# Performance work log

Hardware: AMD Instinct MI355X
Metric: run time of the kernel (lower is better)

Reference implementation:

```python
import jax, jax.numpy as jnp
import numpy as np

HIP_L, HIP_R = 11, 12          # hip joint indices along V
K_LIST = (2, 3, 4, 5)          # soft-selector kNN MoE k values
TAU = 0.35                     # tau_center for ball softmax
EPS = 1e-6


def _sym_norm(A):
    # D^{-1/2} A D^{-1/2} without materializing diag matrices
    d = A.sum(-1)
    dis = jax.lax.rsqrt(d + EPS)
    return dis[..., :, None] * A * dis[..., None, :]


def _knn_adj(pos, k):
    # pos: (N, M, 3) -> 0/1 kNN adjacency (+I self loop, diag ends up 2 as in torch ref)
    M = pos.shape[1]
    diff = pos[:, :, None, :] - pos[:, None, :, :]
    d = jnp.sqrt(jnp.sum(diff * diff, axis=-1))  # (N, M, M) euclidean cdist
    idx = jax.lax.top_k(-d, k)[1]                # (N, M, k) k smallest distances (incl. self)
    A = jax.nn.one_hot(idx, M, dtype=pos.dtype).sum(2)  # scatter 1.0 at kNN columns
    return A + jnp.eye(M, dtype=pos.dtype)


def setup_inputs() -> dict:
    key = jax.random.key(0)
    k1, k2 = jax.random.split(key)
    N, C, T, V, M = 64, 8, 300, 17, 12
    x = jax.random.normal(k1, (N, C, T, V, M), jnp.float32)
    alpha_logits = jax.random.normal(k2, (len(K_LIST),), jnp.float32) * 0.1
    lambda_fuse = jnp.array([0.1], jnp.float32)
    tag_gate = jnp.array([1.0], jnp.float32)
    return {"x": x, "alpha_logits": alpha_logits,
            "lambda_fuse": lambda_fuse, "tag_gate": tag_gate}


def reference(x, alpha_logits, lambda_fuse, tag_gate):
    N, C, T, V, M = x.shape
    # hip-root position averaged over time: (N, M, 3)
    root3 = 0.5 * (x[:, 0:3, :, HIP_L, :] + x[:, 0:3, :, HIP_R, :])  # (N,3,T,M)
    pos = root3.mean(2).transpose(0, 2, 1)                           # (N,M,3)

    # kNN mixture-of-graphs, sym-normalized, detached (detach_adj=True)
    A_knn_stack = jnp.stack([_sym_norm(_knn_adj(pos, k)) for k in K_LIST], 1)  # (N,K,M,M)
    A_knn_stack = jax.lax.stop_gradient(A_knn_stack)
    alpha = jax.nn.softmax(alpha_logits)          # global selector, temp=1
    A_knn = jnp.einsum('k,nkij->nij', alpha, A_knn_stack)

    # soft ball-star graph
    s = x[:, 3].mean((1, 2))                      # (N,M) ball score
    p = jax.nn.softmax(s / TAU, axis=1)
    A_ball = p[:, :, None] + p[:, None, :] + jnp.eye(M, dtype=x.dtype)
    A_ball = jax.lax.stop_gradient(_sym_norm(A_ball))

    # adaptive ball weight from confidence of p (NOT detached)
    w = jnp.clip((jnp.max(p, 1, keepdims=True) - 1.0 / M) / (1.0 - 1.0 / M + EPS), 0.0, 1.0)
    A = w[:, :, None] * A_ball + (1.0 - w[:, :, None]) * A_knn  # (N,M,M)

    # message passing across persons on hip-root features, fused back residually
    root = 0.5 * (x[:, :, :, HIP_L, :] + x[:, :, :, HIP_R, :])  # (N,C,T,M)
    agg = jnp.einsum('nuv,nctv->nctu', A, root)                 # (N,C,T,M)
    g = jnp.tanh(tag_gate[0])  # ramp=1 (ramp_epochs=0), gate_max=1
    return x + g * lambda_fuse[0] * (agg - root)[:, :, :, None, :]
```

## Files before the change

### kernel.cpp

```cpp
#include <hip/hip_runtime.h>
#include <math.h>

#define N_ 64
#define C_ 8
#define T_ 300
#define V_ 17
#define M_ 12
#define EPSF 1e-6f
#define TAUF 0.35f

typedef float f32x4 __attribute__((ext_vector_type(4)));


#define TSPLIT 20
#define TCH (T_ / TSPLIT)

__global__ __launch_bounds__(256) void k_reduce(const float* __restrict__ x,
                                                float* __restrict__ ws_part) {
    const int n = blockIdx.x;
    const int by = blockIdx.y;
    const int t0 = by * TCH;
    const int tid = threadIdx.x;
    __shared__ float pos_acc[36];
    __shared__ float s_acc[12];
    if (tid < 36) pos_acc[tid] = 0.f;
    if (tid < 12) s_acc[tid] = 0.f;
    __syncthreads();

    {
        const f32x4* xs4 = (const f32x4*)(x + ((size_t)(n * C_ + 3) * T_ + t0) * 204);
        f32x4 a0 = {0.f, 0.f, 0.f, 0.f}, a1 = a0, a2 = a0;
        #pragma unroll
        for (int k = 0; k < 3; ++k) {
            int f = tid + 256 * k;
            if (f < TCH * 51) {
                f32x4 v = xs4[f];
                if (k == 0) a0 += v;
                else if (k == 1) a1 += v;
                else a2 += v;
            }
        }
        int mb0 = (4 * tid) % 12;
        int mb1 = (4 * (tid + 1)) % 12;
        int mb2 = (4 * (tid + 2)) % 12;
        #pragma unroll
        for (int c = 0; c < 4; ++c) {
            atomicAdd(&s_acc[mb0 + c], a0[c]);
            atomicAdd(&s_acc[mb1 + c], a1[c]);
            atomicAdd(&s_acc[mb2 + c], a2[c]);
        }
    }

    for (int e = tid; e < 3 * TCH * 6; e += 256) {
        int d = e / (TCH * 6);
        int rem = e % (TCH * 6);
        int tt = rem / 6, q = rem % 6;
        const f32x4* xp4 = (const f32x4*)(x + ((size_t)(n * C_ + d) * T_ + t0 + tt) * 204 + 132);
        f32x4 v = xp4[q];
        int m0 = (q % 3) * 4;
        atomicAdd(&pos_acc[d * 12 + m0 + 0], v.x);
        atomicAdd(&pos_acc[d * 12 + m0 + 1], v.y);
        atomicAdd(&pos_acc[d * 12 + m0 + 2], v.z);
        atomicAdd(&pos_acc[d * 12 + m0 + 3], v.w);
    }
    __syncthreads();

    float* slot = ws_part + (size_t)(n * TSPLIT + by) * 48;
    if (tid < 36) slot[tid] = pos_acc[tid];
    if (tid < 12) slot[36 + tid] = s_acc[tid];
}

#define RT 30
__global__ __launch_bounds__(256) void k_main(const float* __restrict__ x,
                                              const float* __restrict__ ws_part,
                                              const float* __restrict__ alpha_logits,
                                              const float* __restrict__ lambda_fuse,
                                              const float* __restrict__ tag_gate,
                                              float* __restrict__ out) {
    const int n = blockIdx.y;
    const int r0 = blockIdx.x * RT;
    const int tid = threadIdx.x;
    __shared__ f32x4 xs4[RT * 51];
    __shared__ float Ash[144];
    __shared__ float delta_sh[RT * 12];
    __shared__ float raw[48];
    __shared__ float posx[12], posy[12], posz[12];
    __shared__ float dist[144];
    __shared__ int ord[60];
    __shared__ float p_s[12];
    __shared__ float alpha_s[4];
    __shared__ float w_s;
    float* xs = (float*)xs4;

    const float* xn = x + (size_t)n * 2400 * 204;
    float* on = out + (size_t)n * 2400 * 204;
    const f32x4* x4 = (const f32x4*)(xn + (size_t)r0 * 204);
    f32x4* o4 = (f32x4*)(on + (size_t)r0 * 204);

    for (int f = tid; f < RT * 51; f += 256) xs4[f] = x4[f];

    if (tid < 48) {
        float a = 0.f;
        #pragma unroll
        for (int j = 0; j < TSPLIT; ++j) a += ws_part[(size_t)(n * TSPLIT + j) * 48 + tid];
        raw[tid] = a;
    }
    float scale = tanhf(tag_gate[0]) * lambda_fuse[0];
    __syncthreads();

    const float PSC = 0.5f / (float)T_;
    if (tid < 12) {
        posx[tid] = raw[0 * 12 + tid] * PSC;
        posy[tid] = raw[1 * 12 + tid] * PSC;
        posz[tid] = raw[2 * 12 + tid] * PSC;
    }
    if (tid == 0) {
        float l0 = alpha_logits[0], l1 = alpha_logits[1], l2 = alpha_logits[2], l3 = alpha_logits[3];
        float mx = fmaxf(fmaxf(l0, l1), fmaxf(l2, l3));
        float e0 = expf(l0 - mx), e1 = expf(l1 - mx), e2 = expf(l2 - mx), e3 = expf(l3 - mx);
        float s = e0 + e1 + e2 + e3;
        alpha_s[0] = e0 / s; alpha_s[1] = e1 / s; alpha_s[2] = e2 / s; alpha_s[3] = e3 / s;
    }
    if (tid == 64) {
        const float SSC = 1.f / ((float)(T_ * V_) * TAUF);
        float sv[12];
        float mx = -1e30f;
        #pragma unroll
        for (int m = 0; m < 12; ++m) { sv[m] = raw[36 + m] * SSC; mx = fmaxf(mx, sv[m]); }
        float sum = 0.f;
        #pragma unroll
        for (int m = 0; m < 12; ++m) { sv[m] = expf(sv[m] - mx); sum += sv[m]; }
        float maxp = 0.f;
        #pragma unroll
        for (int m = 0; m < 12; ++m) { sv[m] = sv[m] / sum; p_s[m] = sv[m]; maxp = fmaxf(maxp, sv[m]); }
        float w = (maxp - 1.f / 12.f) / (1.f - 1.f / 12.f + EPSF);
        w_s = fminf(fmaxf(w, 0.f), 1.f);
    }
    __syncthreads();

    if (tid < 144) {
        int i = tid / 12, j = tid % 12;
        float dx = posx[i] - posx[j], dy = posy[i] - posy[j], dz = posz[i] - posz[j];
        dist[tid] = sqrtf(dx * dx + dy * dy + dz * dz);
    }
    __syncthreads();

    if (tid < 12) {
        int i = tid, mask = 0;
        #pragma unroll
        for (int r = 0; r < 5; ++r) {
            float bd = 1e30f; int bj = -1;
            #pragma unroll
            for (int j = 0; j < 12; ++j) {
                if (!((mask >> j) & 1)) {
                    float dd = dist[i * 12 + j];
                    if (dd < bd) { bd = dd; bj = j; }
                }
            }
            ord[i * 5 + r] = bj; mask |= (1 << bj);
        }
    }
    __syncthreads();

    if (tid < 144) {
        int i = tid / 12, j = tid % 12;
        int rank = 5;
        #pragma unroll
        for (int r = 4; r >= 0; --r) if (ord[i * 5 + r] == j) rank = r;
        float diag = (i == j) ? 1.f : 0.f;
        float aknn = 0.f;
        #pragma unroll
        for (int kk = 0; kk < 4; ++kk) {
            int K = kk + 2;
            float val = ((rank < K) ? 1.f : 0.f) + diag;
            aknn += alpha_s[kk] * val / ((float)(K + 1) + EPSF);
        }
        float pi = p_s[i], pj = p_s[j];
        float di = 12.f * pi + 2.f, dj = 12.f * pj + 2.f;
        float ab = (pi + pj + diag) * rsqrtf(di + EPSF) * rsqrtf(dj + EPSF);
        float w = w_s;
        Ash[tid] = w * ab + (1.f - w) * aknn;
    }
    __syncthreads();

    for (int e = tid; e < RT * 12; e += 256) {
        int r = e / 12, u = e % 12;
        const float* row = xs + r * 204;
        float acc = 0.f;
        #pragma unroll
        for (int v = 0; v < 12; ++v) {
            float rv = 0.5f * (row[132 + v] + row[144 + v]);
            acc += Ash[u * 12 + v] * rv;
        }
        float ru = 0.5f * (row[132 + u] + row[144 + u]);
        delta_sh[e] = scale * (acc - ru);
    }
    __syncthreads();

    for (int f = tid; f < RT * 51; f += 256) {
        int r = f / 51, j = f % 51;
        int m0 = (4 * j) % 12;
        f32x4 v = xs4[f];
        const float* d = &delta_sh[r * 12 + m0];
        v.x += d[0]; v.y += d[1]; v.z += d[2]; v.w += d[3];
        __builtin_nontemporal_store(v, &o4[f]);
    }
}

extern "C" void kernel_launch(void* const* d_in, const int* in_sizes, int n_in,
                              void* d_out, int out_size, void* d_ws, size_t ws_size,
                              hipStream_t stream) {
    const float* x = (const float*)d_in[0];
    const float* alpha_logits = (const float*)d_in[1];
    const float* lambda_fuse = (const float*)d_in[2];
    const float* tag_gate = (const float*)d_in[3];
    float* out = (float*)d_out;

    float* ws_part = (float*)d_ws;

    k_reduce<<<dim3(N_, TSPLIT), dim3(256), 0, stream>>>(x, ws_part);
    k_main<<<dim3(2400 / RT, N_), dim3(256), 0, stream>>>(x, ws_part, alpha_logits,
                                                          lambda_fuse, tag_gate, out);
}
```

Measured before the change: 256.2 us.

## Split main kernel into per-row delta kernel and grid-stride streaming add

When workspace allows, the fused per-tile kernel is replaced by two launches. The first builds the adjacency once per block of 240 rows and writes a 12-wide delta per (n,c,t) row to workspace. The second is a grid-stride streaming kernel that reads x, adds the delta and stores the output. This aims to cut the repeated per-30-row adjacency construction and the shared-memory staging, at the cost of an extra launch, a global delta round-trip, and strided hip-joint reads in the delta kernel.

```diff
diff --git a/kernel.cpp b/kernel.cpp
--- a/kernel.cpp
+++ b/kernel.cpp
@@ -70,13 +70,162 @@
     if (tid < 12) slot[36 + tid] = s_acc[tid];
 }
 
+__device__ __forceinline__ void build_A(const float* __restrict__ ws_part,
+                                        const float* __restrict__ alpha_logits,
+                                        int n, int tid,
+                                        float* Ash, float* raw,
+                                        float* posx, float* posy, float* posz,
+                                        float* dist, int* ord, float* p_s,
+                                        float* alpha_s, float* w_s) {
+    if (tid < 48) {
+        float a = 0.f;
+        #pragma unroll
+        for (int j = 0; j < TSPLIT; ++j) a += ws_part[(size_t)(n * TSPLIT + j) * 48 + tid];
+        raw[tid] = a;
+    }
+    __syncthreads();
+
+    const float PSC = 0.5f / (float)T_;
+    if (tid < 12) {
+        posx[tid] = raw[0 * 12 + tid] * PSC;
+        posy[tid] = raw[1 * 12 + tid] * PSC;
+        posz[tid] = raw[2 * 12 + tid] * PSC;
+    }
+    if (tid == 0) {
+        float l0 = alpha_logits[0], l1 = alpha_logits[1], l2 = alpha_logits[2], l3 = alpha_logits[3];
+        float mx = fmaxf(fmaxf(l0, l1), fmaxf(l2, l3));
+        float e0 = expf(l0 - mx), e1 = expf(l1 - mx), e2 = expf(l2 - mx), e3 = expf(l3 - mx);
+        float s = e0 + e1 + e2 + e3;
+        alpha_s[0] = e0 / s; alpha_s[1] = e1 / s; alpha_s[2] = e2 / s; alpha_s[3] = e3 / s;
+    }
+    if (tid == 64) {
+        const float SSC = 1.f / ((float)(T_ * V_) * TAUF);
+        float sv[12];
+        float mx = -1e30f;
+        #pragma unroll
+        for (int m = 0; m < 12; ++m) { sv[m] = raw[36 + m] * SSC; mx = fmaxf(mx, sv[m]); }
+        float sum = 0.f;
+        #pragma unroll
+        for (int m = 0; m < 12; ++m) { sv[m] = expf(sv[m] - mx); sum += sv[m]; }
+        float maxp = 0.f;
+        #pragma unroll
+        for (int m = 0; m < 12; ++m) { sv[m] = sv[m] / sum; p_s[m] = sv[m]; maxp = fmaxf(maxp, sv[m]); }
+        float w = (maxp - 1.f / 12.f) / (1.f - 1.f / 12.f + EPSF);
+        *w_s = fminf(fmaxf(w, 0.f), 1.f);
+    }
+    __syncthreads();
+
+    if (tid < 144) {
+        int i = tid / 12, j = tid % 12;
+        float dx = posx[i] - posx[j], dy = posy[i] - posy[j], dz = posz[i] - posz[j];
+        dist[tid] = sqrtf(dx * dx + dy * dy + dz * dz);
+    }
+    __syncthreads();
+
+    if (tid < 12) {
+        int i = tid, mask = 0;
+        #pragma unroll
+        for (int r = 0; r < 5; ++r) {
+            float bd = 1e30f; int bj = -1;
+            #pragma unroll
+            for (int j = 0; j < 12; ++j) {
+                if (!((mask >> j) & 1)) {
+                    float dd = dist[i * 12 + j];
+                    if (dd < bd) { bd = dd; bj = j; }
+                }
+            }
+            ord[i * 5 + r] = bj; mask |= (1 << bj);
+        }
+    }
+    __syncthreads();
+
+    if (tid < 144) {
+        int i = tid / 12, j = tid % 12;
+        int rank = 5;
+        #pragma unroll
+        for (int r = 4; r >= 0; --r) if (ord[i * 5 + r] == j) rank = r;
+        float diag = (i == j) ? 1.f : 0.f;
+        float aknn = 0.f;
+        #pragma unroll
+        for (int kk = 0; kk < 4; ++kk) {
+            int K = kk + 2;
+            float val = ((rank < K) ? 1.f : 0.f) + diag;
+            aknn += alpha_s[kk] * val / ((float)(K + 1) + EPSF);
+        }
+        float pi = p_s[i], pj = p_s[j];
+        float di = 12.f * pi + 2.f, dj = 12.f * pj + 2.f;
+        float ab = (pi + pj + diag) * rsqrtf(di + EPSF) * rsqrtf(dj + EPSF);
+        float w = *w_s;
+        Ash[tid] = w * ab + (1.f - w) * aknn;
+    }
+    __syncthreads();
+}
+
+#define RD 240
+__global__ __launch_bounds__(256) void k_delta(const float* __restrict__ x,
+                                               const float* __restrict__ ws_part,
+                                               const float* __restrict__ alpha_logits,
+                                               const float* __restrict__ lambda_fuse,
+                                               const float* __restrict__ tag_gate,
+                                               float* __restrict__ ws_delta) {
+    const int n = blockIdx.y;
+    const int r0 = blockIdx.x * RD;
+    const int tid = threadIdx.x;
+    __shared__ float Ash[144];
+    __shared__ float raw[48];
+    __shared__ float posx[12], posy[12], posz[12];
+    __shared__ float dist[144];
+    __shared__ int ord[60];
+    __shared__ float p_s[12];
+    __shared__ float alpha_s[4];
+    __shared__ float w_s;
+
+    build_A(ws_part, alpha_logits, n, tid, Ash, raw, posx, posy, posz, dist, ord, p_s, alpha_s, &w_s);
+    float scale = tanhf(tag_gate[0]) * lambda_fuse[0];
+
+    const float* xn = x + (size_t)n * 2400 * 204;
+    float* dn = ws_delta + ((size_t)n * 2400 + r0) * 12;
+
+    for (int r = tid; r < RD; r += 256) {
+        const float* row = xn + (size_t)(r0 + r) * 204;
+        float rt[12];
+        #pragma unroll
+        for (int v = 0; v < 12; ++v) rt[v] = 0.5f * (row[132 + v] + row[144 + v]);
+        #pragma unroll
+        for (int u = 0; u < 12; ++u) {
+            float acc = 0.f;
+            #pragma unroll
+            for (int v = 0; v < 12; ++v) acc += Ash[u * 12 + v] * rt[v];
+            dn[r * 12 + u] = scale * (acc - rt[u]);
+        }
+    }
+}
+
+__global__ __launch_bounds__(256) void k_stream(const float* __restrict__ x,
+                                                const float* __restrict__ ws_delta,
+                                                float* __restrict__ out) {
+    const size_t F = (size_t)N_ * 2400 * 51;
+    const f32x4* x4 = (const f32x4*)x;
+    f32x4* o4 = (f32x4*)out;
+    size_t stride = (size_t)gridDim.x * 256;
+    for (size_t f = (size_t)blockIdx.x * 256 + threadIdx.x; f < F; f += stride) {
+        size_t gr = f / 51;
+        int j = (int)(f - gr * 51);
+        int m0 = (4 * j) % 12;
+        f32x4 v = x4[f];
+        const f32x4 d = *(const f32x4*)(ws_delta + gr * 12 + m0);
+        v.x += d.x; v.y += d.y; v.z += d.z; v.w += d.w;
+        __builtin_nontemporal_store(v, &o4[f]);
+    }
+}
+
 #define RT 30
-__global__ __launch_bounds__(256) void k_main(const float* __restrict__ x,
-                                              const float* __restrict__ ws_part,
-                                              const float* __restrict__ alpha_logits,
-                                              const float* __restrict__ lambda_fuse,
-                                              const float* __restrict__ tag_gate,
-                                              float* __restrict__ out) {
+__global__ __launch_bounds__(256) void k_main_fused(const float* __restrict__ x,
+                                                    const float* __restrict__ ws_part,
+                                                    const float* __restrict__ alpha_logits,
+                                                    const float* __restrict__ lambda_fuse,
+                                                    const float* __restrict__ tag_gate,
+                                                    float* __restrict__ out) {
     const int n = blockIdx.y;
     const int r0 = blockIdx.x * RT;
     const int tid = threadIdx.x;
@@ -98,89 +247,8 @@
     f32x4* o4 = (f32x4*)(on + (size_t)r0 * 204);
 
     for (int f = tid; f < RT * 51; f += 256) xs4[f] = x4[f];
-
-    if (tid < 48) {
-        float a = 0.f;
-        #pragma unroll
-        for (int j = 0; j < TSPLIT; ++j) a += ws_part[(size_t)(n * TSPLIT + j) * 48 + tid];
-        raw[tid] = a;
-    }
+    build_A(ws_part, alpha_logits, n, tid, Ash, raw, posx, posy, posz, dist, ord, p_s, alpha_s, &w_s);
     float scale = tanhf(tag_gate[0]) * lambda_fuse[0];
-    __syncthreads();
-
-    const float PSC = 0.5f / (float)T_;
-    if (tid < 12) {
-        posx[tid] = raw[0 * 12 + tid] * PSC;
-        posy[tid] = raw[1 * 12 + tid] * PSC;
-        posz[tid] = raw[2 * 12 + tid] * PSC;
-    }
-    if (tid == 0) {
-        float l0 = alpha_logits[0], l1 = alpha_logits[1], l2 = alpha_logits[2], l3 = alpha_logits[3];
-        float mx = fmaxf(fmaxf(l0, l1), fmaxf(l2, l3));
-        float e0 = expf(l0 - mx), e1 = expf(l1 - mx), e2 = expf(l2 - mx), e3 = expf(l3 - mx);
-        float s = e0 + e1 + e2 + e3;
-        alpha_s[0] = e0 / s; alpha_s[1] = e1 / s; alpha_s[2] = e2 / s; alpha_s[3] = e3 / s;
-    }
-    if (tid == 64) {
-        const float SSC = 1.f / ((float)(T_ * V_) * TAUF);
-        float sv[12];
-        float mx = -1e30f;
-        #pragma unroll
-        for (int m = 0; m < 12; ++m) { sv[m] = raw[36 + m] * SSC; mx = fmaxf(mx, sv[m]); }
-        float sum = 0.f;
-        #pragma unroll
-        for (int m = 0; m < 12; ++m) { sv[m] = expf(sv[m] - mx); sum += sv[m]; }
-        float maxp = 0.f;
-        #pragma unroll
-        for (int m = 0; m < 12; ++m) { sv[m] = sv[m] / sum; p_s[m] = sv[m]; maxp = fmaxf(maxp, sv[m]); }
-        float w = (maxp - 1.f / 12.f) / (1.f - 1.f / 12.f + EPSF);
-        w_s = fminf(fmaxf(w, 0.f), 1.f);
-    }
-    __syncthreads();
-
-    if (tid < 144) {
-        int i = tid / 12, j = tid % 12;
-        float dx = posx[i] - posx[j], dy = posy[i] - posy[j], dz = posz[i] - posz[j];
-        dist[tid] = sqrtf(dx * dx + dy * dy + dz * dz);
-    }
-    __syncthreads();
-
-    if (tid < 12) {
-        int i = tid, mask = 0;
-        #pragma unroll
-        for (int r = 0; r < 5; ++r) {
-            float bd = 1e30f; int bj = -1;
-            #pragma unroll
-            for (int j = 0; j < 12; ++j) {
-                if (!((mask >> j) & 1)) {
-                    float dd = dist[i * 12 + j];
-                    if (dd < bd) { bd = dd; bj = j; }
-                }
-            }
-            ord[i * 5 + r] = bj; mask |= (1 << bj);
-        }
-    }
-    __syncthreads();
-
-    if (tid < 144) {
-        int i = tid / 12, j = tid % 12;
-        int rank = 5;
-        #pragma unroll
-        for (int r = 4; r >= 0; --r) if (ord[i * 5 + r] == j) rank = r;
-        float diag = (i == j) ? 1.f : 0.f;
-        float aknn = 0.f;
-        #pragma unroll
-        for (int kk = 0; kk < 4; ++kk) {
-            int K = kk + 2;
-            float val = ((rank < K) ? 1.f : 0.f) + diag;
-            aknn += alpha_s[kk] * val / ((float)(K + 1) + EPSF);
-        }
-        float pi = p_s[i], pj = p_s[j];
-        float di = 12.f * pi + 2.f, dj = 12.f * pj + 2.f;
-        float ab = (pi + pj + diag) * rsqrtf(di + EPSF) * rsqrtf(dj + EPSF);
-        float w = w_s;
-        Ash[tid] = w * ab + (1.f - w) * aknn;
-    }
     __syncthreads();
 
     for (int e = tid; e < RT * 12; e += 256) {
@@ -216,9 +284,18 @@
     const float* tag_gate = (const float*)d_in[3];
     float* out = (float*)d_out;
 
-    float* ws_part = (float*)d_ws;
+    float* ws = (float*)d_ws;
+    float* ws_part = ws;
+    float* ws_delta = ws + 64 * TSPLIT * 48;
+    const size_t need = ((size_t)64 * TSPLIT * 48 + (size_t)64 * 2400 * 12) * sizeof(float);
 
     k_reduce<<<dim3(N_, TSPLIT), dim3(256), 0, stream>>>(x, ws_part);
-    k_main<<<dim3(2400 / RT, N_), dim3(256), 0, stream>>>(x, ws_part, alpha_logits,
-                                                          lambda_fuse, tag_gate, out);
-}
+    if (ws_size >= need) {
+        k_delta<<<dim3(2400 / RD, N_), dim3(256), 0, stream>>>(x, ws_part, alpha_logits,
+                                                               lambda_fuse, tag_gate, ws_delta);
+        k_stream<<<dim3(2048), dim3(256), 0, stream>>>(x, ws_delta, out);
+    } else {
+        k_main_fused<<<dim3(2400 / RT, N_), dim3(256), 0, stream>>>(x, ws_part, alpha_logits,
+                                                                    lambda_fuse, tag_gate, out);
+    }
+}
```

Result: no change. 259.7 us (+1.4%).
